# Optimization experiments

Measured on AMD Instinct MI355X. Metric: run time of the kernel, lower is better.

## Reference

```python
import jax, jax.numpy as jnp
import numpy as np
from jax import lax

SHARED = 512
THRESH = 1.0   # LifNeuron threshold from source
DECAY = 0.9    # assumed LIF membrane decay (LifNeuron source not provided)


def spike(u):
    return (u >= 0.0).astype(u.dtype)


def lif(x):
    # Leaky integrate-and-fire over the time axis. x: (B, T, D) -> spikes (B, T, D)
    def step(mem, xt):
        mem = DECAY * mem + xt
        s = spike(mem - THRESH)
        return mem - s * THRESH, s
    x_t = jnp.swapaxes(x, 0, 1)  # (T, B, D)
    _, spikes = lax.scan(step, jnp.zeros((x.shape[0], x.shape[2]), x.dtype), x_t)
    return jnp.swapaxes(spikes, 0, 1)


def setup_inputs() -> dict:
    key = jax.random.key(0)
    ks = jax.random.split(key, 10)
    B, T, S = 2, 32, 64
    Dv, Da = 768, 512
    TENSOR_DIM = (SHARED + 1) ** 2  # 263169

    def lin_w(k, fan_in, fan_out):
        # torch.nn.Linear default init scale ~ 1/sqrt(fan_in)
        return (jax.random.normal(k, (fan_out, fan_in), jnp.float32)
                * np.float32(1.0 / np.sqrt(fan_in)))

    return {
        "vision": jax.random.uniform(ks[0], (B, T, S, Dv), jnp.float32),
        "audio": jax.random.uniform(ks[1], (B, T, S, Da), jnp.float32),
        "vw1": lin_w(ks[2], Dv, SHARED), "vb1": jnp.zeros((SHARED,), jnp.float32),
        "vw2": lin_w(ks[3], SHARED, SHARED), "vb2": jnp.zeros((SHARED,), jnp.float32),
        "aw1": lin_w(ks[4], Da, SHARED), "ab1": jnp.zeros((SHARED,), jnp.float32),
        "aw2": lin_w(ks[5], SHARED, SHARED), "ab2": jnp.zeros((SHARED,), jnp.float32),
        "fw1": lin_w(ks[6], TENSOR_DIM, 2 * SHARED), "fb1": jnp.zeros((2 * SHARED,), jnp.float32),
        "fw2": lin_w(ks[7], 2 * SHARED, SHARED), "fb2": jnp.zeros((SHARED,), jnp.float32),
    }


def reference(vision, audio, vw1, vb1, vw2, vb2, aw1, ab1, aw2, ab2,
              fw1, fb1, fw2, fb2):
    def unimodal(x, w1, b1, w2, b2):
        p = x.mean(axis=2)  # (B, T, D_mod) - pool over spike/token axis
        h = jax.nn.relu(jnp.einsum('btd,hd->bth', p, w1) + b1)
        h = jnp.einsum('bth,oh->bto', h, w2) + b2  # (B, T, SHARED)
        ones = jnp.ones(h.shape[:-1] + (1,), h.dtype)
        return jnp.concatenate([h, ones], axis=-1)  # (B, T, SHARED+1)

    a = unimodal(vision, vw1, vb1, vw2, vb2)
    b = unimodal(audio, aw1, ab1, aw2, ab2)
    B, T, _ = a.shape
    # outer-product tensor fusion: (B, T, (SHARED+1)^2)
    tp = jnp.einsum('btd,bte->btde', a, b).reshape(B, T, -1)
    h = jax.nn.relu(jnp.einsum('btk,ok->bto', tp, fw1) + fb1)
    fused = jnp.einsum('bto,fo->btf', h, fw2) + fb2  # (B, T, SHARED)
    return lif(fused)
```

## Files before the change

kernel.cpp:

```cpp
#include <hip/hip_runtime.h>

#define AB 513
#define TD 263169

typedef float f4 __attribute__((ext_vector_type(4)));
typedef float f32x4 __attribute__((ext_vector_type(4)));
typedef short bf16x8 __attribute__((ext_vector_type(8)));
typedef int i32x4 __attribute__((ext_vector_type(4)));
#define GAS __attribute__((address_space(1)))
#define LAS __attribute__((address_space(3)))

__global__ __launch_bounds__(256) void pool_kernel(
    const float* __restrict__ vx, const float* __restrict__ ax,
    float* __restrict__ pvT, float* __restrict__ paT)
{
    const int isA = (blockIdx.x >= 64);
    const int bt = blockIdx.x & 63;
    const float* x = isA ? ax : vx;
    float* pT = isA ? paT : pvT;
    const int D = isA ? 512 : 768;
    const int nd4 = D >> 2;
    const int tid = threadIdx.x;
    if (tid < nd4) {
        f4 s0 = {0.f, 0.f, 0.f, 0.f}, s1 = s0, s2 = s0, s3 = s0;
        const float* xp = x + (size_t)bt * 64 * D + tid * 4;
        #pragma unroll 4
        for (int ss = 0; ss < 64; ss += 4) {
            s0 += *(const f4*)(xp + (size_t)ss * D);
            s1 += *(const f4*)(xp + (size_t)(ss + 1) * D);
            s2 += *(const f4*)(xp + (size_t)(ss + 2) * D);
            s3 += *(const f4*)(xp + (size_t)(ss + 3) * D);
        }
        const f4 s = ((s0 + s1) + (s2 + s3)) * 0.015625f;
        #pragma unroll
        for (int q = 0; q < 4; ++q) pT[(tid * 4 + q) * 64 + bt] = s[q];
    }
}

__global__ __launch_bounds__(512) void mlp1_kernel(
    const float* __restrict__ pvT, const float* __restrict__ paT,
    const float* __restrict__ vw1, const float* __restrict__ vb1,
    const float* __restrict__ aw1, const float* __restrict__ ab1,
    float* __restrict__ h1vT, float* __restrict__ h1aT)
{
    const int isA = (blockIdx.x >= 64);
    const int D = isA ? 512 : 768;
    const float* pT = isA ? paT : pvT;
    const float* w1 = isA ? aw1 : vw1;
    const float* b1 = isA ? ab1 : vb1;
    float* h1T = isA ? h1aT : h1vT;
    const int tid = threadIdx.x, lane = tid & 63, w = tid >> 6;
    const int h = (blockIdx.x & 63) * 8 + w;
    const float* wr = w1 + (size_t)h * D;

    float a0 = 0.f, a1 = 0.f, a2 = 0.f, a3 = 0.f;
    for (int d = 0; d < D; d += 16) {
        const f4 w0 = *(const f4*)(wr + d);
        const f4 w1v = *(const f4*)(wr + d + 4);
        const f4 w2v = *(const f4*)(wr + d + 8);
        const f4 w3v = *(const f4*)(wr + d + 12);
        #pragma unroll
        for (int q = 0; q < 4; ++q) {
            a0 = fmaf(w0[q],  pT[(d + q) * 64 + lane], a0);
            a1 = fmaf(w1v[q], pT[(d + 4 + q) * 64 + lane], a1);
            a2 = fmaf(w2v[q], pT[(d + 8 + q) * 64 + lane], a2);
            a3 = fmaf(w3v[q], pT[(d + 12 + q) * 64 + lane], a3);
        }
    }
    h1T[h * 64 + lane] = fmaxf((a0 + a1) + (a2 + a3) + b1[h], 0.f);
}

__global__ __launch_bounds__(512) void mlp2_kernel(
    const float* __restrict__ h1vT, const float* __restrict__ h1aT,
    const float* __restrict__ vw2, const float* __restrict__ vb2,
    const float* __restrict__ aw2, const float* __restrict__ ab2,
    float* __restrict__ aTout, float* __restrict__ bTout)
{
    const int isA = (blockIdx.x >= 64);
    const float* hT = isA ? h1aT : h1vT;
    const float* w2 = isA ? aw2 : vw2;
    const float* b2 = isA ? ab2 : vb2;
    float* outT = isA ? bTout : aTout;
    const int tid = threadIdx.x, lane = tid & 63, w = tid >> 6;
    const int h = (blockIdx.x & 63) * 8 + w;
    const float* wr = w2 + (size_t)h * 512;

    float a0 = 0.f, a1 = 0.f, a2 = 0.f, a3 = 0.f;
    for (int d = 0; d < 512; d += 16) {
        const f4 w0 = *(const f4*)(wr + d);
        const f4 w1v = *(const f4*)(wr + d + 4);
        const f4 w2v = *(const f4*)(wr + d + 8);
        const f4 w3v = *(const f4*)(wr + d + 12);
        #pragma unroll
        for (int q = 0; q < 4; ++q) {
            a0 = fmaf(w0[q],  hT[(d + q) * 64 + lane], a0);
            a1 = fmaf(w1v[q], hT[(d + 4 + q) * 64 + lane], a1);
            a2 = fmaf(w2v[q], hT[(d + 8 + q) * 64 + lane], a2);
            a3 = fmaf(w3v[q], hT[(d + 12 + q) * 64 + lane], a3);
        }
    }
    outT[h * 64 + lane] = (a0 + a1) + (a2 + a3) + b2[h];
    if ((blockIdx.x & 63) == 0 && tid < 64) outT[512 * 64 + tid] = 1.0f;
}

__global__ __launch_bounds__(256) void aprep_kernel(
    const float* __restrict__ aT,
    short* __restrict__ aF1, short* __restrict__ aF2, short* __restrict__ aF3)
{
    const int t = blockIdx.x * 256 + threadIdx.x;
    const int l = t & 63, mt = (t >> 6) & 3, kt = t >> 8;
    const int m = mt * 16 + (l & 15);
    const int kbase = kt * 32 + ((l >> 4) << 3);
    const int obase = ((kt * 4 + mt) * 64 + l) * 8;
    #pragma unroll
    for (int i = 0; i < 8; ++i) {
        const float v = aT[(size_t)(kbase + i) * 64 + m];
        const unsigned u = __float_as_uint(v);
        const float r1 = v - __uint_as_float(u & 0xFFFF0000u);
        const unsigned u1 = __float_as_uint(r1);
        const float r2 = r1 - __uint_as_float(u1 & 0xFFFF0000u);
        const unsigned u2 = __float_as_uint(r2);
        aF1[obase + i] = (short)(u >> 16);
        aF2[obase + i] = (short)(u1 >> 16);
        aF3[obase + i] = (short)(u2 >> 16);
    }
}

__global__ __launch_bounds__(512, 1) void bilinear_kernel(
    const float* __restrict__ fw1,
    const float* __restrict__ fb1,
    const float* __restrict__ aT,
    const float* __restrict__ bT,
    const short* __restrict__ aF1, const short* __restrict__ aF2,
    const short* __restrict__ aF3,
    float* __restrict__ hbufT)
{
    __shared__ float ring[8][2][2048];
    const int tid = threadIdx.x;
    const int l = tid & 63, w = tid >> 6;
    const int o = blockIdx.x;
    const float* __restrict__ W = fw1 + (size_t)o * TD;
    const int we0 = w * 64;
    const int lq = l >> 4, ln = l & 15;
    float* const myring = &ring[w][0][0];

    #define STAGE(buf_, kt_)                                                   \
        do {                                                                   \
            _Pragma("unroll")                                                  \
            for (int is_ = 0; is_ < 8; ++is_) {                                \
                const int g_ = is_ * 64 + l;                                   \
                const int row_ = g_ >> 4, c4_ = (g_ & 15) * 4;                 \
                __builtin_amdgcn_global_load_lds(                              \
                    (const GAS unsigned*)(const void*)(W + (size_t)((kt_) * 32 + row_) * AB + we0 + c4_), \
                    (LAS unsigned*)(void*)(myring + (buf_) * 2048 + is_ * 256 + l * 4), 16, 0, 0); \
            }                                                                  \
        } while (0)

    #define LOADA(A1r, A2r, A3r, kt_)                                          \
        do {                                                                   \
            _Pragma("unroll")                                                  \
            for (int mt_ = 0; mt_ < 4; ++mt_) {                                \
                const int fb_ = (((kt_) * 4 + mt_) * 64 + l) * 8;              \
                A1r[mt_] = *(const bf16x8*)(aF1 + fb_);                        \
                A2r[mt_] = *(const bf16x8*)(aF2 + fb_);                        \
                A3r[mt_] = *(const bf16x8*)(aF3 + fb_);                        \
            }                                                                  \
        } while (0)

    #define COMPUTE(kt_, A1r, A2r, A3r)                                        \
        do {                                                                   \
            const float* __restrict__ wb_ = myring + ((kt_) & 1) * 2048;       \
            _Pragma("unroll")                                                  \
            for (int nt = 0; nt < 4; ++nt) {                                   \
                unsigned u0[8], u1[8], u2[8];                                  \
                _Pragma("unroll")                                              \
                for (int i = 0; i < 8; ++i) {                                  \
                    const float v = wb_[(lq * 8 + i) * 64 + nt * 16 + ln];     \
                    u0[i] = __float_as_uint(v);                                \
                    const float r1 = v - __uint_as_float(u0[i] & 0xFFFF0000u); \
                    u1[i] = __float_as_uint(r1);                               \
                    const float r2 = r1 - __uint_as_float(u1[i] & 0xFFFF0000u);\
                    u2[i] = __float_as_uint(r2);                               \
                }                                                              \
                i32x4 p1, p2, p3;                                              \
                _Pragma("unroll")                                              \
                for (int j = 0; j < 4; ++j) {                                  \
                    p1[j] = (int)((u0[2 * j + 1] & 0xFFFF0000u) | (u0[2 * j] >> 16)); \
                    p2[j] = (int)((u1[2 * j + 1] & 0xFFFF0000u) | (u1[2 * j] >> 16)); \
                    p3[j] = (int)((u2[2 * j + 1] & 0xFFFF0000u) | (u2[2 * j] >> 16)); \
                }                                                              \
                const bf16x8 B1 = __builtin_bit_cast(bf16x8, p1);              \
                const bf16x8 B2 = __builtin_bit_cast(bf16x8, p2);              \
                const bf16x8 B3 = __builtin_bit_cast(bf16x8, p3);              \
                _Pragma("unroll")                                              \
                for (int mt = 0; mt < 4; ++mt) {                               \
                    acc[mt][nt] = __builtin_amdgcn_mfma_f32_16x16x32_bf16(A1r[mt], B1, acc[mt][nt], 0, 0, 0); \
                    acc[mt][nt] = __builtin_amdgcn_mfma_f32_16x16x32_bf16(A1r[mt], B2, acc[mt][nt], 0, 0, 0); \
                    acc[mt][nt] = __builtin_amdgcn_mfma_f32_16x16x32_bf16(A2r[mt], B1, acc[mt][nt], 0, 0, 0); \
                    acc[mt][nt] = __builtin_amdgcn_mfma_f32_16x16x32_bf16(A2r[mt], B2, acc[mt][nt], 0, 0, 0); \
                    acc[mt][nt] = __builtin_amdgcn_mfma_f32_16x16x32_bf16(A1r[mt], B3, acc[mt][nt], 0, 0, 0); \
                    acc[mt][nt] = __builtin_amdgcn_mfma_f32_16x16x32_bf16(A3r[mt], B1, acc[mt][nt], 0, 0, 0); \
                }                                                              \
            }                                                                  \
        } while (0)

    f32x4 acc[4][4];
    #pragma unroll
    for (int mt = 0; mt < 4; ++mt)
        #pragma unroll
        for (int nt = 0; nt < 4; ++nt)
            acc[mt][nt] = (f32x4){0.f, 0.f, 0.f, 0.f};

    bf16x8 Aa1[4], Aa2[4], Aa3[4], Ab1[4], Ab2[4], Ab3[4];

    STAGE(0, 0);
    LOADA(Aa1, Aa2, Aa3, 0);
    STAGE(1, 1);

    #pragma unroll 1
    for (int it = 0; it < 7; ++it) {
        const int kt = 2 * it;
        asm volatile("s_waitcnt vmcnt(8)" ::: "memory");
        LOADA(Ab1, Ab2, Ab3, kt + 1);
        COMPUTE(kt, Aa1, Aa2, Aa3);
        asm volatile("" ::: "memory");
        STAGE(kt & 1, kt + 2);

        asm volatile("s_waitcnt vmcnt(8)" ::: "memory");
        LOADA(Aa1, Aa2, Aa3, kt + 2);
        COMPUTE(kt + 1, Ab1, Ab2, Ab3);
        asm volatile("" ::: "memory");
        STAGE((kt + 1) & 1, kt + 3);
    }
    asm volatile("s_waitcnt vmcnt(8)" ::: "memory");
    LOADA(Ab1, Ab2, Ab3, 15);
    COMPUTE(14, Aa1, Aa2, Aa3);
    asm volatile("s_waitcnt vmcnt(0)" ::: "memory");
    COMPUTE(15, Ab1, Ab2, Ab3);

    float ysum[4][4];
    #pragma unroll
    for (int mt = 0; mt < 4; ++mt)
        #pragma unroll
        for (int r = 0; r < 4; ++r) ysum[mt][r] = 0.f;
    #pragma unroll
    for (int mt = 0; mt < 4; ++mt) {
        const int bt0 = mt * 16 + lq * 4;
        #pragma unroll
        for (int nt = 0; nt < 4; ++nt) {
            const int e = we0 + nt * 16 + ln;
            const f4 bv = *(const f4*)(bT + (size_t)e * 64 + bt0);
            #pragma unroll
            for (int r = 0; r < 4; ++r)
                ysum[mt][r] = fmaf(acc[mt][nt][r], bv[r], ysum[mt][r]);
        }
    }
    #pragma unroll
    for (int mt = 0; mt < 4; ++mt)
        #pragma unroll
        for (int r = 0; r < 4; ++r) {
            float v = ysum[mt][r];
            v += __shfl_xor(v, 1, 64);
            v += __shfl_xor(v, 2, 64);
            v += __shfl_xor(v, 4, 64);
            v += __shfl_xor(v, 8, 64);
            ysum[mt][r] = v;
        }
    if (ln == 0) {
        #pragma unroll
        for (int mt = 0; mt < 4; ++mt)
            #pragma unroll
            for (int r = 0; r < 4; ++r)
                myring[mt * 16 + lq * 4 + r] = ysum[mt][r];
    }

    {
        float s0 = 0.f, s1 = 0.f, s2 = 0.f, s3 = 0.f;
        #pragma unroll 4
        for (int k = 0; k < 64; k += 4) {
            s0 = fmaf(aT[(size_t)(we0 + k) * 64 + l], W[(size_t)(we0 + k) * AB + 512], s0);
            s1 = fmaf(aT[(size_t)(we0 + k + 1) * 64 + l], W[(size_t)(we0 + k + 1) * AB + 512], s1);
            s2 = fmaf(aT[(size_t)(we0 + k + 2) * 64 + l], W[(size_t)(we0 + k + 2) * AB + 512], s2);
            s3 = fmaf(aT[(size_t)(we0 + k + 3) * 64 + l], W[(size_t)(we0 + k + 3) * AB + 512], s3);
        }
        #pragma unroll 4
        for (int k = 0; k < 64; k += 4) {
            s0 = fmaf(W[(size_t)512 * AB + we0 + k], bT[(size_t)(we0 + k) * 64 + l], s0);
            s1 = fmaf(W[(size_t)512 * AB + we0 + k + 1], bT[(size_t)(we0 + k + 1) * 64 + l], s1);
            s2 = fmaf(W[(size_t)512 * AB + we0 + k + 2], bT[(size_t)(we0 + k + 2) * 64 + l], s2);
            s3 = fmaf(W[(size_t)512 * AB + we0 + k + 3], bT[(size_t)(we0 + k + 3) * 64 + l], s3);
        }
        myring[64 + l] = (s0 + s1) + (s2 + s3);
    }

    __syncthreads();

    if (w == 0) {
        float t2 = 0.f;
        #pragma unroll
        for (int k = 0; k < 8; ++k)
            t2 += ring[k][0][l] + ring[k][0][64 + l];
        t2 += W[(size_t)512 * AB + 512] + fb1[o];
        hbufT[(size_t)o * 64 + l] = fmaxf(t2, 0.f);
    }
    #undef STAGE
    #undef LOADA
    #undef COMPUTE
}

__global__ __launch_bounds__(512) void fuse2_kernel(
    const float* __restrict__ hbufT,
    const float* __restrict__ fw2,
    const float* __restrict__ fb2,
    float* __restrict__ fused)
{
    const int tid = threadIdx.x, lane = tid & 63, w = tid >> 6;
    #pragma unroll
    for (int k = 0; k < 2; ++k) {
        const int f = blockIdx.x * 16 + w * 2 + k;
        const float* wr = fw2 + (size_t)f * 1024;
        float a0 = 0.f, a1 = 0.f, a2 = 0.f, a3 = 0.f;
        for (int o = 0; o < 1024; o += 16) {
            const f4 w0 = *(const f4*)(wr + o);
            const f4 w1v = *(const f4*)(wr + o + 4);
            const f4 w2v = *(const f4*)(wr + o + 8);
            const f4 w3v = *(const f4*)(wr + o + 12);
            #pragma unroll
            for (int q = 0; q < 4; ++q) {
                a0 = fmaf(w0[q],  hbufT[(o + q) * 64 + lane], a0);
                a1 = fmaf(w1v[q], hbufT[(o + 4 + q) * 64 + lane], a1);
                a2 = fmaf(w2v[q], hbufT[(o + 8 + q) * 64 + lane], a2);
                a3 = fmaf(w3v[q], hbufT[(o + 12 + q) * 64 + lane], a3);
            }
        }
        fused[lane * 512 + f] = (a0 + a1) + (a2 + a3) + fb2[f];
    }
}

__global__ __launch_bounds__(256) void lif_kernel(
    const float* __restrict__ fused,
    float* __restrict__ out)
{
    const int idx = blockIdx.x * 256 + threadIdx.x;
    if (idx >= 1024) return;
    const int b = idx >> 9, dd = idx & 511;
    float mem = 0.f;
    for (int t = 0; t < 32; ++t) {
        const size_t off = ((size_t)(b * 32 + t) * 512) + dd;
        mem = 0.9f * mem + fused[off];
        const float s = (mem >= 1.0f) ? 1.0f : 0.0f;
        out[off] = s;
        mem -= s;
    }
}

extern "C" void kernel_launch(void* const* d_in, const int* in_sizes, int n_in,
                              void* d_out, int out_size, void* d_ws, size_t ws_size,
                              hipStream_t stream) {
    const float* vision = (const float*)d_in[0];
    const float* audio  = (const float*)d_in[1];
    const float* vw1 = (const float*)d_in[2];
    const float* vb1 = (const float*)d_in[3];
    const float* vw2 = (const float*)d_in[4];
    const float* vb2 = (const float*)d_in[5];
    const float* aw1 = (const float*)d_in[6];
    const float* ab1 = (const float*)d_in[7];
    const float* aw2 = (const float*)d_in[8];
    const float* ab2 = (const float*)d_in[9];
    const float* fw1 = (const float*)d_in[10];
    const float* fb1 = (const float*)d_in[11];
    const float* fw2 = (const float*)d_in[12];
    const float* fb2 = (const float*)d_in[13];
    float* out = (float*)d_out;

    float* ws    = (float*)d_ws;
    float* pvT   = ws;
    float* paT   = pvT + 768 * 64;
    float* h1vT  = paT + 512 * 64;
    float* h1aT  = h1vT + 512 * 64;
    float* aT    = h1aT + 512 * 64;
    float* bT    = aT + AB * 64;
    float* hbufT = bT + AB * 64;
    float* fused = hbufT + 1024 * 64;
    short* aF1   = (short*)(fused + 64 * 512);
    short* aF2   = aF1 + 32768;
    short* aF3   = aF2 + 32768;

    pool_kernel<<<128, 256, 0, stream>>>(vision, audio, pvT, paT);
    mlp1_kernel<<<128, 512, 0, stream>>>(pvT, paT, vw1, vb1, aw1, ab1, h1vT, h1aT);
    mlp2_kernel<<<128, 512, 0, stream>>>(h1vT, h1aT, vw2, vb2, aw2, ab2, aT, bT);
    aprep_kernel<<<16, 256, 0, stream>>>(aT, aF1, aF2, aF3);
    bilinear_kernel<<<1024, 512, 0, stream>>>(fw1, fb1, aT, bT, aF1, aF2, aF3, hbufT);
    fuse2_kernel<<<32, 512, 0, stream>>>(hbufT, fw2, fb2, fused);
    lif_kernel<<<4, 256, 0, stream>>>(fused, out);
}
```

Before: 417.7 us.

## Stage contiguous 32-row weight chunks into shared LDS with block-wide barriers

Each weight chunk of 32 full rows (32×513 floats) is now copied contiguously into a block-shared LDS double buffer. Previously each wave gathered its own 64-column slice with strided row addresses into a private ring. The contiguous loads are meant to improve global coalescing and DRAM streaming of the large fw1 matrix. The cost is that all waves now share each buffer, so s_barrier calls are needed around compute and staging. That couples the waves, and the 513-float row stride may cause LDS bank conflicts.

```diff
diff --git a/kernel.cpp b/kernel.cpp
--- a/kernel.cpp
+++ b/kernel.cpp
@@ -2,6 +2,7 @@
 
 #define AB 513
 #define TD 263169
+#define TILE 16416
 
 typedef float f4 __attribute__((ext_vector_type(4)));
 typedef float f32x4 __attribute__((ext_vector_type(4)));
@@ -135,24 +136,33 @@
     const short* __restrict__ aF3,
     float* __restrict__ hbufT)
 {
-    __shared__ float ring[8][2][2048];
+    __shared__ float lds[33344];
+    float* const buf0 = lds;
+    float* const buf1 = lds + 16448;
+    float* const ldsdump = lds + 32896;
+
     const int tid = threadIdx.x;
     const int l = tid & 63, w = tid >> 6;
     const int o = blockIdx.x;
     const float* __restrict__ W = fw1 + (size_t)o * TD;
     const int we0 = w * 64;
     const int lq = l >> 4, ln = l & 15;
-    float* const myring = &ring[w][0][0];
-
-    #define STAGE(buf_, kt_)                                                   \
+
+    #define STAGE(bufb_, c_)                                                   \
         do {                                                                   \
+            const float* csrc_ = W + (size_t)(c_) * TILE;                      \
             _Pragma("unroll")                                                  \
             for (int is_ = 0; is_ < 8; ++is_) {                                \
-                const int g_ = is_ * 64 + l;                                   \
-                const int row_ = g_ >> 4, c4_ = (g_ & 15) * 4;                 \
                 __builtin_amdgcn_global_load_lds(                              \
-                    (const GAS unsigned*)(const void*)(W + (size_t)((kt_) * 32 + row_) * AB + we0 + c4_), \
-                    (LAS unsigned*)(void*)(myring + (buf_) * 2048 + is_ * 256 + l * 4), 16, 0, 0); \
+                    (const GAS unsigned*)(const void*)(csrc_ + w * 2048 + is_ * 256 + l * 4), \
+                    (LAS unsigned*)(void*)((bufb_) + w * 2048 + is_ * 256), 16, 0, 0); \
+            }                                                                  \
+            {       \
+                const float* rs_ = csrc_ + 16384 + (l & 31);                   \
+                float* rd_ = (w == 0) ? ((bufb_) + 16384) : (ldsdump + (w - 1) * 64); \
+                __builtin_amdgcn_global_load_lds(                              \
+                    (const GAS unsigned*)(const void*)rs_,                     \
+                    (LAS unsigned*)(void*)rd_, 4, 0, 0);                       \
             }                                                                  \
         } while (0)
 
@@ -167,15 +177,14 @@
             }                                                                  \
         } while (0)
 
-    #define COMPUTE(kt_, A1r, A2r, A3r)                                        \
+    #define COMPUTE(wb_, A1r, A2r, A3r)                                        \
         do {                                                                   \
-            const float* __restrict__ wb_ = myring + ((kt_) & 1) * 2048;       \
             _Pragma("unroll")                                                  \
             for (int nt = 0; nt < 4; ++nt) {                                   \
                 unsigned u0[8], u1[8], u2[8];                                  \
                 _Pragma("unroll")                                              \
                 for (int i = 0; i < 8; ++i) {                                  \
-                    const float v = wb_[(lq * 8 + i) * 64 + nt * 16 + ln];     \
+                    const float v = (wb_)[(lq * 8 + i) * 513 + we0 + nt * 16 + ln]; \
                     u0[i] = __float_as_uint(v);                                \
                     const float r1 = v - __uint_as_float(u0[i] & 0xFFFF0000u); \
                     u1[i] = __float_as_uint(r1);                               \
@@ -213,30 +222,34 @@
 
     bf16x8 Aa1[4], Aa2[4], Aa3[4], Ab1[4], Ab2[4], Ab3[4];
 
-    STAGE(0, 0);
+    STAGE(buf0, 0);
     LOADA(Aa1, Aa2, Aa3, 0);
-    STAGE(1, 1);
+    STAGE(buf1, 1);
 
     #pragma unroll 1
     for (int it = 0; it < 7; ++it) {
-        const int kt = 2 * it;
-        asm volatile("s_waitcnt vmcnt(8)" ::: "memory");
-        LOADA(Ab1, Ab2, Ab3, kt + 1);
-        COMPUTE(kt, Aa1, Aa2, Aa3);
-        asm volatile("" ::: "memory");
-        STAGE(kt & 1, kt + 2);
-
-        asm volatile("s_waitcnt vmcnt(8)" ::: "memory");
-        LOADA(Aa1, Aa2, Aa3, kt + 2);
-        COMPUTE(kt + 1, Ab1, Ab2, Ab3);
-        asm volatile("" ::: "memory");
-        STAGE((kt + 1) & 1, kt + 3);
-    }
-    asm volatile("s_waitcnt vmcnt(8)" ::: "memory");
+        asm volatile("s_waitcnt vmcnt(9)" ::: "memory");
+        __builtin_amdgcn_s_barrier();
+        LOADA(Ab1, Ab2, Ab3, 2 * it + 1);
+        COMPUTE(buf0, Aa1, Aa2, Aa3);
+        __builtin_amdgcn_s_barrier();
+        STAGE(buf0, 2 * it + 2);
+
+        asm volatile("s_waitcnt vmcnt(9)" ::: "memory");
+        __builtin_amdgcn_s_barrier();
+        LOADA(Aa1, Aa2, Aa3, 2 * it + 2);
+        COMPUTE(buf1, Ab1, Ab2, Ab3);
+        __builtin_amdgcn_s_barrier();
+        STAGE(buf1, 2 * it + 3);
+    }
+    asm volatile("s_waitcnt vmcnt(9)" ::: "memory");
+    __builtin_amdgcn_s_barrier();
     LOADA(Ab1, Ab2, Ab3, 15);
-    COMPUTE(14, Aa1, Aa2, Aa3);
+    COMPUTE(buf0, Aa1, Aa2, Aa3);
+    __builtin_amdgcn_s_barrier();
     asm volatile("s_waitcnt vmcnt(0)" ::: "memory");
-    COMPUTE(15, Ab1, Ab2, Ab3);
+    __builtin_amdgcn_s_barrier();
+    COMPUTE(buf1, Ab1, Ab2, Ab3);
 
     float ysum[4][4];
     #pragma unroll
@@ -266,12 +279,13 @@
             v += __shfl_xor(v, 8, 64);
             ysum[mt][r] = v;
         }
+    __syncthreads();
     if (ln == 0) {
         #pragma unroll
         for (int mt = 0; mt < 4; ++mt)
             #pragma unroll
             for (int r = 0; r < 4; ++r)
-                myring[mt * 16 + lq * 4 + r] = ysum[mt][r];
+                buf0[w * 64 + mt * 16 + lq * 4 + r] = ysum[mt][r];
     }
 
     {
@@ -290,7 +304,7 @@
             s2 = fmaf(W[(size_t)512 * AB + we0 + k + 2], bT[(size_t)(we0 + k + 2) * 64 + l], s2);
             s3 = fmaf(W[(size_t)512 * AB + we0 + k + 3], bT[(size_t)(we0 + k + 3) * 64 + l], s3);
         }
-        myring[64 + l] = (s0 + s1) + (s2 + s3);
+        buf0[512 + w * 64 + l] = (s0 + s1) + (s2 + s3);
     }
 
     __syncthreads();
@@ -299,7 +313,7 @@
         float t2 = 0.f;
         #pragma unroll
         for (int k = 0; k < 8; ++k)
-            t2 += ring[k][0][l] + ring[k][0][64 + l];
+            t2 += buf0[k * 64 + l] + buf0[512 + k * 64 + l];
         t2 += W[(size_t)512 * AB + 512] + fb1[o];
         hbufT[(size_t)o * 64 + l] = fmaxf(t2, 0.f);
     }
```

Result: no change. 423.2 us (+1.3%).

## Split bilinear kernel over two column halves with shared LDS staging and 2 blocks/CU

Applied to the files above, without the earlier changes.

Each output row o of fw1 is now handled by two blocks, each covering half of the 512 e-columns. Within a block, waves share a padded (257-stride) LDS tile via barriers instead of private per-wave rings, and each wave computes 2 m-tiles × 4 n-tiles. Launch bounds allow 2 blocks per CU. Partial sums go to two buffers, and the bias plus ReLU combine moves into fuse2. The aim is more occupancy and better latency hiding on the memory-bound fw1 stream, at the cost of extra block barriers and extra partial-sum traffic.

```diff
diff --git a/kernel.cpp b/kernel.cpp
--- a/kernel.cpp
+++ b/kernel.cpp
@@ -126,56 +126,55 @@
     }
 }
 
-__global__ __launch_bounds__(512, 1) void bilinear_kernel(
+__global__ __launch_bounds__(512, 2) void bilinear_kernel(
     const float* __restrict__ fw1,
-    const float* __restrict__ fb1,
     const float* __restrict__ aT,
     const float* __restrict__ bT,
     const short* __restrict__ aF1, const short* __restrict__ aF2,
     const short* __restrict__ aF3,
-    float* __restrict__ hbufT)
-{
-    __shared__ float ring[8][2][2048];
+    float* __restrict__ hp0,
+    float* __restrict__ hp1)
+{
+    __shared__ float lds[2][8224];
     const int tid = threadIdx.x;
     const int l = tid & 63, w = tid >> 6;
-    const int o = blockIdx.x;
+    const int o = blockIdx.x >> 1, eh = blockIdx.x & 1;
     const float* __restrict__ W = fw1 + (size_t)o * TD;
-    const int we0 = w * 64;
+    const int bh = w >> 2, ew = w & 3;
     const int lq = l >> 4, ln = l & 15;
-    float* const myring = &ring[w][0][0];
 
     #define STAGE(buf_, kt_)                                                   \
         do {                                                                   \
             _Pragma("unroll")                                                  \
-            for (int is_ = 0; is_ < 8; ++is_) {                                \
-                const int g_ = is_ * 64 + l;                                   \
-                const int row_ = g_ >> 4, c4_ = (g_ & 15) * 4;                 \
+            for (int r_ = 0; r_ < 4; ++r_) {                                   \
+                const int row_ = w * 4 + r_;                                   \
                 __builtin_amdgcn_global_load_lds(                              \
-                    (const GAS unsigned*)(const void*)(W + (size_t)((kt_) * 32 + row_) * AB + we0 + c4_), \
-                    (LAS unsigned*)(void*)(myring + (buf_) * 2048 + is_ * 256 + l * 4), 16, 0, 0); \
+                    (const GAS unsigned*)(const void*)(W + (size_t)((kt_) * 32 + row_) * AB + 256 * eh + l * 4), \
+                    (LAS unsigned*)(void*)(&lds[buf_][row_ * 257]), 16, 0, 0); \
             }                                                                  \
         } while (0)
 
-    #define LOADA(A1r, A2r, A3r, kt_)                                          \
+    #define LOADA(kt_)                                                         \
         do {                                                                   \
             _Pragma("unroll")                                                  \
-            for (int mt_ = 0; mt_ < 4; ++mt_) {                                \
-                const int fb_ = (((kt_) * 4 + mt_) * 64 + l) * 8;              \
-                A1r[mt_] = *(const bf16x8*)(aF1 + fb_);                        \
-                A2r[mt_] = *(const bf16x8*)(aF2 + fb_);                        \
-                A3r[mt_] = *(const bf16x8*)(aF3 + fb_);                        \
+            for (int mi_ = 0; mi_ < 2; ++mi_) {                                \
+                const int fb_ = (((kt_) * 4 + (2 * bh + mi_)) * 64 + l) * 8;   \
+                A1[mi_] = *(const bf16x8*)(aF1 + fb_);                         \
+                A2[mi_] = *(const bf16x8*)(aF2 + fb_);                         \
+                A3[mi_] = *(const bf16x8*)(aF3 + fb_);                         \
             }                                                                  \
         } while (0)
 
-    #define COMPUTE(kt_, A1r, A2r, A3r)                                        \
+    #define COMPUTE(buf_)                                                      \
         do {                                                                   \
-            const float* __restrict__ wb_ = myring + ((kt_) & 1) * 2048;       \
+            const float* __restrict__ wb_ = &lds[buf_][0];                     \
             _Pragma("unroll")                                                  \
             for (int nt = 0; nt < 4; ++nt) {                                   \
+                const int ecol_ = 64 * ew + nt * 16 + ln;                      \
                 unsigned u0[8], u1[8], u2[8];                                  \
                 _Pragma("unroll")                                              \
                 for (int i = 0; i < 8; ++i) {                                  \
-                    const float v = wb_[(lq * 8 + i) * 64 + nt * 16 + ln];     \
+                    const float v = wb_[(lq * 8 + i) * 257 + ecol_];           \
                     u0[i] = __float_as_uint(v);                                \
                     const float r1 = v - __uint_as_float(u0[i] & 0xFFFF0000u); \
                     u1[i] = __float_as_uint(r1);                               \
@@ -193,115 +192,123 @@
                 const bf16x8 B2 = __builtin_bit_cast(bf16x8, p2);              \
                 const bf16x8 B3 = __builtin_bit_cast(bf16x8, p3);              \
                 _Pragma("unroll")                                              \
-                for (int mt = 0; mt < 4; ++mt) {                               \
-                    acc[mt][nt] = __builtin_amdgcn_mfma_f32_16x16x32_bf16(A1r[mt], B1, acc[mt][nt], 0, 0, 0); \
-                    acc[mt][nt] = __builtin_amdgcn_mfma_f32_16x16x32_bf16(A1r[mt], B2, acc[mt][nt], 0, 0, 0); \
-                    acc[mt][nt] = __builtin_amdgcn_mfma_f32_16x16x32_bf16(A2r[mt], B1, acc[mt][nt], 0, 0, 0); \
-                    acc[mt][nt] = __builtin_amdgcn_mfma_f32_16x16x32_bf16(A2r[mt], B2, acc[mt][nt], 0, 0, 0); \
-                    acc[mt][nt] = __builtin_amdgcn_mfma_f32_16x16x32_bf16(A1r[mt], B3, acc[mt][nt], 0, 0, 0); \
-                    acc[mt][nt] = __builtin_amdgcn_mfma_f32_16x16x32_bf16(A3r[mt], B1, acc[mt][nt], 0, 0, 0); \
+                for (int mi = 0; mi < 2; ++mi) {                               \
+                    acc[mi][nt] = __builtin_amdgcn_mfma_f32_16x16x32_bf16(A1[mi], B1, acc[mi][nt], 0, 0, 0); \
+                    acc[mi][nt] = __builtin_amdgcn_mfma_f32_16x16x32_bf16(A1[mi], B2, acc[mi][nt], 0, 0, 0); \
+                    acc[mi][nt] = __builtin_amdgcn_mfma_f32_16x16x32_bf16(A2[mi], B1, acc[mi][nt], 0, 0, 0); \
+                    acc[mi][nt] = __builtin_amdgcn_mfma_f32_16x16x32_bf16(A2[mi], B2, acc[mi][nt], 0, 0, 0); \
+                    acc[mi][nt] = __builtin_amdgcn_mfma_f32_16x16x32_bf16(A1[mi], B3, acc[mi][nt], 0, 0, 0); \
+                    acc[mi][nt] = __builtin_amdgcn_mfma_f32_16x16x32_bf16(A3[mi], B1, acc[mi][nt], 0, 0, 0); \
                 }                                                              \
             }                                                                  \
         } while (0)
 
-    f32x4 acc[4][4];
-    #pragma unroll
-    for (int mt = 0; mt < 4; ++mt)
+    f32x4 acc[2][4];
+    #pragma unroll
+    for (int mi = 0; mi < 2; ++mi)
         #pragma unroll
         for (int nt = 0; nt < 4; ++nt)
-            acc[mt][nt] = (f32x4){0.f, 0.f, 0.f, 0.f};
-
-    bf16x8 Aa1[4], Aa2[4], Aa3[4], Ab1[4], Ab2[4], Ab3[4];
+            acc[mi][nt] = (f32x4){0.f, 0.f, 0.f, 0.f};
+    bf16x8 A1[2], A2[2], A3[2];
 
     STAGE(0, 0);
-    LOADA(Aa1, Aa2, Aa3, 0);
+    LOADA(0);
     STAGE(1, 1);
 
     #pragma unroll 1
-    for (int it = 0; it < 7; ++it) {
-        const int kt = 2 * it;
-        asm volatile("s_waitcnt vmcnt(8)" ::: "memory");
-        LOADA(Ab1, Ab2, Ab3, kt + 1);
-        COMPUTE(kt, Aa1, Aa2, Aa3);
-        asm volatile("" ::: "memory");
+    for (int kt = 0; kt < 14; ++kt) {
+        asm volatile("s_waitcnt vmcnt(4)" ::: "memory");
+        __builtin_amdgcn_s_barrier();
+        COMPUTE(kt & 1);
+        LOADA(kt + 1);
+        __builtin_amdgcn_s_barrier();
         STAGE(kt & 1, kt + 2);
-
-        asm volatile("s_waitcnt vmcnt(8)" ::: "memory");
-        LOADA(Aa1, Aa2, Aa3, kt + 2);
-        COMPUTE(kt + 1, Ab1, Ab2, Ab3);
-        asm volatile("" ::: "memory");
-        STAGE((kt + 1) & 1, kt + 3);
-    }
-    asm volatile("s_waitcnt vmcnt(8)" ::: "memory");
-    LOADA(Ab1, Ab2, Ab3, 15);
-    COMPUTE(14, Aa1, Aa2, Aa3);
+    }
+    asm volatile("s_waitcnt vmcnt(4)" ::: "memory");
+    __builtin_amdgcn_s_barrier();
+    COMPUTE(0);
+    LOADA(15);
+    __builtin_amdgcn_s_barrier();
     asm volatile("s_waitcnt vmcnt(0)" ::: "memory");
-    COMPUTE(15, Ab1, Ab2, Ab3);
-
-    float ysum[4][4];
-    #pragma unroll
-    for (int mt = 0; mt < 4; ++mt)
-        #pragma unroll
-        for (int r = 0; r < 4; ++r) ysum[mt][r] = 0.f;
-    #pragma unroll
-    for (int mt = 0; mt < 4; ++mt) {
-        const int bt0 = mt * 16 + lq * 4;
+    __builtin_amdgcn_s_barrier();
+    COMPUTE(1);
+
+    float* const redM = &lds[0][0];
+    float* const redA = &lds[0][256];
+    float* const redC = &lds[0][768];
+
+    float ysum[2][4];
+    #pragma unroll
+    for (int mi = 0; mi < 2; ++mi)
+        #pragma unroll
+        for (int r = 0; r < 4; ++r) ysum[mi][r] = 0.f;
+    #pragma unroll
+    for (int mi = 0; mi < 2; ++mi) {
+        const int bt0 = (2 * bh + mi) * 16 + lq * 4;
         #pragma unroll
         for (int nt = 0; nt < 4; ++nt) {
-            const int e = we0 + nt * 16 + ln;
+            const int e = 256 * eh + 64 * ew + nt * 16 + ln;
             const f4 bv = *(const f4*)(bT + (size_t)e * 64 + bt0);
             #pragma unroll
             for (int r = 0; r < 4; ++r)
-                ysum[mt][r] = fmaf(acc[mt][nt][r], bv[r], ysum[mt][r]);
-        }
-    }
-    #pragma unroll
-    for (int mt = 0; mt < 4; ++mt)
+                ysum[mi][r] = fmaf(acc[mi][nt][r], bv[r], ysum[mi][r]);
+        }
+    }
+    #pragma unroll
+    for (int mi = 0; mi < 2; ++mi)
         #pragma unroll
         for (int r = 0; r < 4; ++r) {
-            float v = ysum[mt][r];
+            float v = ysum[mi][r];
             v += __shfl_xor(v, 1, 64);
             v += __shfl_xor(v, 2, 64);
             v += __shfl_xor(v, 4, 64);
             v += __shfl_xor(v, 8, 64);
-            ysum[mt][r] = v;
+            ysum[mi][r] = v;
         }
     if (ln == 0) {
         #pragma unroll
-        for (int mt = 0; mt < 4; ++mt)
+        for (int mi = 0; mi < 2; ++mi)
             #pragma unroll
             for (int r = 0; r < 4; ++r)
-                myring[mt * 16 + lq * 4 + r] = ysum[mt][r];
+                redM[w * 32 + mi * 16 + lq * 4 + r] = ysum[mi][r];
     }
 
     {
-        float s0 = 0.f, s1 = 0.f, s2 = 0.f, s3 = 0.f;
+        float s = 0.f;
         #pragma unroll 4
-        for (int k = 0; k < 64; k += 4) {
-            s0 = fmaf(aT[(size_t)(we0 + k) * 64 + l], W[(size_t)(we0 + k) * AB + 512], s0);
-            s1 = fmaf(aT[(size_t)(we0 + k + 1) * 64 + l], W[(size_t)(we0 + k + 1) * AB + 512], s1);
-            s2 = fmaf(aT[(size_t)(we0 + k + 2) * 64 + l], W[(size_t)(we0 + k + 2) * AB + 512], s2);
-            s3 = fmaf(aT[(size_t)(we0 + k + 3) * 64 + l], W[(size_t)(we0 + k + 3) * AB + 512], s3);
-        }
+        for (int j = 0; j < 32; ++j) {
+            const int e = 256 * eh + 32 * w + j;
+            s = fmaf(W[(size_t)512 * AB + e], bT[(size_t)e * 64 + l], s);
+        }
+        redA[w * 64 + l] = s;
+    }
+    if (eh == 0) {
+        float s = 0.f;
         #pragma unroll 4
-        for (int k = 0; k < 64; k += 4) {
-            s0 = fmaf(W[(size_t)512 * AB + we0 + k], bT[(size_t)(we0 + k) * 64 + l], s0);
-            s1 = fmaf(W[(size_t)512 * AB + we0 + k + 1], bT[(size_t)(we0 + k + 1) * 64 + l], s1);
-            s2 = fmaf(W[(size_t)512 * AB + we0 + k + 2], bT[(size_t)(we0 + k + 2) * 64 + l], s2);
-            s3 = fmaf(W[(size_t)512 * AB + we0 + k + 3], bT[(size_t)(we0 + k + 3) * 64 + l], s3);
-        }
-        myring[64 + l] = (s0 + s1) + (s2 + s3);
+        for (int k = 0; k < 64; ++k) {
+            const int d = 64 * w + k;
+            s = fmaf(aT[(size_t)d * 64 + l], W[(size_t)d * AB + 512], s);
+        }
+        redC[w * 64 + l] = s;
     }
 
     __syncthreads();
 
     if (w == 0) {
-        float t2 = 0.f;
-        #pragma unroll
-        for (int k = 0; k < 8; ++k)
-            t2 += ring[k][0][l] + ring[k][0][64 + l];
-        t2 += W[(size_t)512 * AB + 512] + fb1[o];
-        hbufT[(size_t)o * 64 + l] = fmaxf(t2, 0.f);
+        const int bh2 = l >> 5, btl = l & 31;
+        float t = 0.f;
+        #pragma unroll
+        for (int e2 = 0; e2 < 4; ++e2) t += redM[(bh2 * 4 + e2) * 32 + btl];
+        #pragma unroll
+        for (int w2 = 0; w2 < 8; ++w2) t += redA[w2 * 64 + l];
+        if (eh == 0) {
+            #pragma unroll
+            for (int w2 = 0; w2 < 8; ++w2) t += redC[w2 * 64 + l];
+            t += W[(size_t)512 * AB + 512];
+            hp0[(size_t)o * 64 + l] = t;
+        } else {
+            hp1[(size_t)o * 64 + l] = t;
+        }
     }
     #undef STAGE
     #undef LOADA
@@ -309,7 +316,9 @@
 }
 
 __global__ __launch_bounds__(512) void fuse2_kernel(
-    const float* __restrict__ hbufT,
+    const float* __restrict__ hp0,
+    const float* __restrict__ hp1,
+    const float* __restrict__ fb1,
     const float* __restrict__ fw2,
     const float* __restrict__ fb2,
     float* __restrict__ fused)
@@ -327,10 +336,15 @@
             const f4 w3v = *(const f4*)(wr + o + 12);
             #pragma unroll
             for (int q = 0; q < 4; ++q) {
-                a0 = fmaf(w0[q],  hbufT[(o + q) * 64 + lane], a0);
-                a1 = fmaf(w1v[q], hbufT[(o + 4 + q) * 64 + lane], a1);
-                a2 = fmaf(w2v[q], hbufT[(o + 8 + q) * 64 + lane], a2);
-                a3 = fmaf(w3v[q], hbufT[(o + 12 + q) * 64 + lane], a3);
+                const int o0 = o + q, o1 = o + 4 + q, o2 = o + 8 + q, o3 = o + 12 + q;
+                const float h0 = fmaxf(hp0[o0 * 64 + lane] + hp1[o0 * 64 + lane] + fb1[o0], 0.f);
+                const float h1 = fmaxf(hp0[o1 * 64 + lane] + hp1[o1 * 64 + lane] + fb1[o1], 0.f);
+                const float h2 = fmaxf(hp0[o2 * 64 + lane] + hp1[o2 * 64 + lane] + fb1[o2], 0.f);
+                const float h3 = fmaxf(hp0[o3 * 64 + lane] + hp1[o3 * 64 + lane] + fb1[o3], 0.f);
+                a0 = fmaf(w0[q], h0, a0);
+                a1 = fmaf(w1v[q], h1, a1);
+                a2 = fmaf(w2v[q], h2, a2);
+                a3 = fmaf(w3v[q], h3, a3);
             }
         }
         fused[lane * 512 + f] = (a0 + a1) + (a2 + a3) + fb2[f];
@@ -380,17 +394,18 @@
     float* h1aT  = h1vT + 512 * 64;
     float* aT    = h1aT + 512 * 64;
     float* bT    = aT + AB * 64;
-    float* hbufT = bT + AB * 64;
-    float* fused = hbufT + 1024 * 64;
+    float* fused = bT + AB * 64;
     short* aF1   = (short*)(fused + 64 * 512);
     short* aF2   = aF1 + 32768;
     short* aF3   = aF2 + 32768;
+    float* hp0   = (float*)(aF3 + 32768);
+    float* hp1   = hp0 + 1024 * 64;
 
     pool_kernel<<<128, 256, 0, stream>>>(vision, audio, pvT, paT);
     mlp1_kernel<<<128, 512, 0, stream>>>(pvT, paT, vw1, vb1, aw1, ab1, h1vT, h1aT);
     mlp2_kernel<<<128, 512, 0, stream>>>(h1vT, h1aT, vw2, vb2, aw2, ab2, aT, bT);
     aprep_kernel<<<16, 256, 0, stream>>>(aT, aF1, aF2, aF3);
-    bilinear_kernel<<<1024, 512, 0, stream>>>(fw1, fb1, aT, bT, aF1, aF2, aF3, hbufT);
-    fuse2_kernel<<<32, 512, 0, stream>>>(hbufT, fw2, fb2, fused);
+    bilinear_kernel<<<2048, 512, 0, stream>>>(fw1, aT, bT, aF1, aF2, aF3, hp0, hp1);
+    fuse2_kernel<<<32, 512, 0, stream>>>(hp0, hp1, fb1, fw2, fb2, fused);
     lif_kernel<<<4, 256, 0, stream>>>(fused, out);
 }
```

Result: slower. 442.8 us (+6.0%).
